# Kernel tuning notes

Measured on AMD Instinct MI355X. Metric: run time of the kernel, lower is better.

Reference implementation:

```python
import jax, jax.numpy as jnp
import numpy as np

B, T, D, H, C, WIN = 2, 2048, 512, 8, 64, 128
EPS = 1e-6


def _rms_norm(x, w):
    # x: (..., C)
    norm = jax.lax.rsqrt(jnp.mean(x * x, axis=-1, keepdims=True) + EPS)
    return x * norm * w


def _apply_rope(x, cos_p, sin_p):
    # x: (B, H, T, C); cos_p/sin_p: (T, C)
    half = x.shape[-1] // 2
    x1, x2 = x[..., :half], x[..., half:]
    rotated = jnp.concatenate([-x2, x1], axis=-1)
    return x * cos_p + rotated * sin_p


def setup_inputs() -> dict:
    key = jax.random.key(0)
    ks = jax.random.split(key, 5)
    h = jax.random.normal(ks[0], (B, T, D), dtype=jnp.float32)
    # RoPE cache (rotate-half convention): (T_max, head_dim)
    inv_freq = 1.0 / (10000.0 ** (jnp.arange(0, C, 2, dtype=jnp.float32) / C))  # (C/2,)
    pos = jnp.arange(T, dtype=jnp.float32)
    freqs = pos[:, None] * inv_freq[None, :]                      # (T, C/2)
    emb = jnp.concatenate([freqs, freqs], axis=-1)                # (T, C)
    rope_cos = jnp.cos(emb)
    rope_sin = jnp.sin(emb)
    scale = 0.02
    W_q = jax.random.normal(ks[1], (D, H * C), dtype=jnp.float32) * scale
    W_k = jax.random.normal(ks[2], (D, H * C), dtype=jnp.float32) * scale
    W_v = jax.random.normal(ks[3], (D, H * C), dtype=jnp.float32) * scale
    W_o = jax.random.normal(ks[4], (H * C, D), dtype=jnp.float32) * scale
    q_norm_w = jnp.ones((C,), dtype=jnp.float32)
    k_norm_w = jnp.ones((C,), dtype=jnp.float32)
    return {"h": h, "rope_cos": rope_cos, "rope_sin": rope_sin,
            "W_q": W_q, "W_k": W_k, "W_v": W_v, "W_o": W_o,
            "q_norm_w": q_norm_w, "k_norm_w": k_norm_w}


def reference(h, rope_cos, rope_sin, W_q, W_k, W_v, W_o, q_norm_w, k_norm_w):
    Bx, Tx, _ = h.shape
    q = (h @ W_q).reshape(Bx, Tx, H, C)
    k = (h @ W_k).reshape(Bx, Tx, H, C)
    v = (h @ W_v).reshape(Bx, Tx, H, C)
    q = _rms_norm(q, q_norm_w)
    k = _rms_norm(k, k_norm_w)
    positions = jnp.arange(Tx)
    cos_p = rope_cos[positions]   # (T, C)
    sin_p = rope_sin[positions]
    # transpose to (B, H, T, C), apply rope, transpose back handled implicitly
    q = _apply_rope(q.transpose(0, 2, 1, 3), cos_p, sin_p).transpose(0, 2, 1, 3)
    k = _apply_rope(k.transpose(0, 2, 1, 3), cos_p, sin_p).transpose(0, 2, 1, 3)
    i = positions[:, None]
    j = positions[None, :]
    sw_mask = (j <= i) & (j > i - WIN)                # (T, T) banded causal
    logits = jnp.einsum('bthc,bshc->bhts', q, k) / np.sqrt(C).astype(np.float32)
    logits = jnp.where(sw_mask[None, None], logits, jnp.float32(-jnp.inf))
    attn = jax.nn.softmax(logits, axis=-1)
    out = jnp.einsum('bhts,bshc->bthc', attn, v).reshape(Bx, Tx, H * C)
    return out @ W_o
```

## Files before the change

kernel.cpp:

```cpp
#include <hip/hip_runtime.h>
#include <hip/hip_bf16.h>
#include <cmath>

#define Bb 2
#define Tt 2048
#define Dd 512
#define Hh 8
#define Cc 64
#define WINw 128

using u16x8 = __attribute__((ext_vector_type(8))) unsigned short;
using s16x8 = __attribute__((ext_vector_type(8))) short;
using f32x4 = __attribute__((ext_vector_type(4))) float;

__device__ __forceinline__ float bf2f(unsigned short u) {
  union { unsigned int i; float f; } v; v.i = ((unsigned int)u) << 16; return v.f;
}
__device__ __forceinline__ unsigned short f2bf(float f) {
  __hip_bfloat16 b = __float2bfloat16(f);
  return *reinterpret_cast<unsigned short*>(&b);
}

#define GLD16(gp, lp)                                                        \
  __builtin_amdgcn_global_load_lds(                                          \
      (const __attribute__((address_space(1))) unsigned int*)(gp),           \
      (__attribute__((address_space(3))) unsigned int*)(lp), 16, 0, 0)

__global__ __launch_bounds__(256) void prep_all(
    const float* __restrict__ s0, const float* __restrict__ s1,
    const float* __restrict__ s2, const float* __restrict__ s3,
    unsigned short* __restrict__ d,
    const float* __restrict__ hsrc, unsigned short* __restrict__ hdst) {
  int tid = threadIdx.x;
  if (blockIdx.z == 4) {
    int gid = ((int)blockIdx.y * 8 + blockIdx.x) * 256 + tid;
    #pragma unroll
    for (int s = 0; s < 16; ++s) {
      size_t i = ((size_t)s * 16384 + gid) * 8;
      const float4* g = (const float4*)&hsrc[i];
      float4 f0 = g[0], f1 = g[1];
      u16x8 o = {f2bf(f0.x), f2bf(f0.y), f2bf(f0.z), f2bf(f0.w),
                 f2bf(f1.x), f2bf(f1.y), f2bf(f1.z), f2bf(f1.w)};
      *(u16x8*)&hdst[i] = o;
    }
    return;
  }
  __shared__ unsigned short tile[64 * 65];
  const float* srcs[4] = {s0, s1, s2, s3};
  const float* src = srcs[blockIdx.z];
  unsigned short* dst = d + (size_t)blockIdx.z * 512 * 512;
  int n0 = blockIdx.x * 64, k0 = blockIdx.y * 64;
  int tx = tid & 63, ty = tid >> 6;
  #pragma unroll
  for (int i = 0; i < 16; ++i) {
    int k = ty * 16 + i;
    tile[k * 65 + tx] = f2bf(src[(k0 + k) * 512 + n0 + tx]);
  }
  __syncthreads();
  #pragma unroll
  for (int i = 0; i < 16; ++i) {
    int n = ty * 16 + i;
    dst[(n0 + n) * 512 + k0 + tx] = tile[tx * 65 + n];
  }
}

__global__ __launch_bounds__(256) void qkv_fused(
    const unsigned short* __restrict__ Hb,
    const unsigned short* __restrict__ WTall,
    const float* __restrict__ qnw, const float* __restrict__ knw,
    const float* __restrict__ rcos, const float* __restrict__ rsin,
    unsigned short* __restrict__ Qw, unsigned short* __restrict__ Kw,
    unsigned short* __restrict__ Vw) {
  __shared__ alignas(16) unsigned short S[12288];
  unsigned short* Al = S;
  unsigned short* Bl = S + 8192;
  int tid = threadIdx.x;
  int wave = tid >> 6, lane = tid & 63;
  int ln = lane & 15, qd = lane >> 4;
  int m0 = blockIdx.x * 128;
  int gh = blockIdx.y;
  int n0 = gh * 64;

  f32x4 acc[2][4];
  #pragma unroll
  for (int mi = 0; mi < 2; ++mi)
    #pragma unroll
    for (int ni = 0; ni < 4; ++ni) acc[mi][ni] = f32x4{0.f, 0.f, 0.f, 0.f};

  for (int k0 = 0; k0 < 512; k0 += 64) {
    #pragma unroll
    for (int s = 0; s < 4; ++s) {
      int q = s * 4 + wave;
      int L = q * 64 + lane;
      int row = L >> 3;
      int cb = (L & 7) ^ (row & 7);
      GLD16(&Hb[(size_t)(m0 + row) * 512 + k0 + cb * 8], (char*)Al + q * 1024);
    }
    #pragma unroll
    for (int s = 0; s < 2; ++s) {
      int q = s * 4 + wave;
      int L = q * 64 + lane;
      int row = L >> 3;
      int cb = (L & 7) ^ (row & 7);
      GLD16(&WTall[(size_t)(n0 + row) * 512 + k0 + cb * 8], (char*)Bl + q * 1024);
    }
    __syncthreads();
    #pragma unroll
    for (int half = 0; half < 2; ++half) {
      s16x8 af[2], bfr[4];
      #pragma unroll
      for (int mi = 0; mi < 2; ++mi) {
        int ar = wave * 32 + mi * 16 + ln;
        int cbp = (qd + half * 4) ^ (ar & 7);
        af[mi] = *(const s16x8*)((const char*)Al + ar * 128 + cbp * 16);
      }
      #pragma unroll
      for (int ni = 0; ni < 4; ++ni) {
        int br = ni * 16 + ln;
        int cbp = (qd + half * 4) ^ (br & 7);
        bfr[ni] = *(const s16x8*)((const char*)Bl + br * 128 + cbp * 16);
      }
      #pragma unroll
      for (int mi = 0; mi < 2; ++mi)
        #pragma unroll
        for (int ni = 0; ni < 4; ++ni)
          acc[mi][ni] = __builtin_amdgcn_mfma_f32_16x16x32_bf16(
              af[mi], bfr[ni], acc[mi][ni], 0, 0, 0);
    }
    __syncthreads();
  }

  int mat = gh >> 3, head = gh & 7;
  const float* nw = (mat == 0) ? qnw : knw;
  bool do_rope = (mat < 2);
  int mrow0 = m0 + wave * 32;
  int b = mrow0 >> 11, tb = mrow0 & (Tt - 1);

  #pragma unroll
  for (int mi = 0; mi < 2; ++mi) {
    float vals[4][4];
    #pragma unroll
    for (int ni = 0; ni < 4; ++ni)
      #pragma unroll
      for (int r = 0; r < 4; ++r) vals[ni][r] = acc[mi][ni][r];

    if (do_rope) {
      #pragma unroll
      for (int r = 0; r < 4; ++r) {
        float ss = 0.f;
        #pragma unroll
        for (int ni = 0; ni < 4; ++ni) ss += vals[ni][r] * vals[ni][r];
        ss += __shfl_xor(ss, 1, 64);
        ss += __shfl_xor(ss, 2, 64);
        ss += __shfl_xor(ss, 4, 64);
        ss += __shfl_xor(ss, 8, 64);
        float nrm = rsqrtf(ss * (1.0f / 64.0f) + 1e-6f);
        #pragma unroll
        for (int ni = 0; ni < 4; ++ni) vals[ni][r] *= nrm;
      }
      #pragma unroll
      for (int ni = 0; ni < 4; ++ni) {
        float w = nw[ni * 16 + ln];
        #pragma unroll
        for (int r = 0; r < 4; ++r) vals[ni][r] *= w;
      }
      float res[4][4];
      #pragma unroll
      for (int r = 0; r < 4; ++r) {
        int t = tb + mi * 16 + qd * 4 + r;
        #pragma unroll
        for (int ni = 0; ni < 4; ++ni) {
          int c = ni * 16 + ln;
          float cs = rcos[t * 64 + c];
          float sn = rsin[t * 64 + c];
          float part = vals[ni ^ 2][r];
          float rot = (ni < 2) ? -part : part;
          res[ni][r] = vals[ni][r] * cs + rot * sn;
        }
      }
      #pragma unroll
      for (int ni = 0; ni < 4; ++ni)
        #pragma unroll
        for (int r = 0; r < 4; ++r) vals[ni][r] = res[ni][r];
    }

    if (mat < 2) {
      unsigned short* Wl = S + wave * 2304;
      #pragma unroll
      for (int ni = 0; ni < 4; ++ni)
        #pragma unroll
        for (int r = 0; r < 4; ++r)
          Wl[(mi * 16 + qd * 4 + r) * 72 + ni * 16 + ln] = f2bf(vals[ni][r]);
    } else {
      unsigned short* Wl = S + wave * 2560;
      #pragma unroll
      for (int ni = 0; ni < 4; ++ni)
        #pragma unroll
        for (int r = 0; r < 4; ++r)
          Wl[(ni * 16 + ln) * 40 + mi * 16 + qd * 4 + r] = f2bf(vals[ni][r]);
    }
  }

  if (mat < 2) {
    unsigned short* Wl = S + wave * 2304;
    unsigned short* Og =
        ((mat == 0) ? Qw : Kw) + (((size_t)b * Hh + head) * Tt + tb) * 64;
    #pragma unroll
    for (int i = 0; i < 4; ++i) {
      int idx = i * 64 + lane;
      int rr = idx >> 3, cc = (idx & 7) * 8;
      *(u16x8*)&Og[rr * 64 + cc] = *(const u16x8*)&Wl[rr * 72 + cc];
    }
  } else {
    unsigned short* Wl = S + wave * 2560;
    unsigned short* Og = Vw + ((size_t)b * Hh + head) * 64 * 2048 + tb;
    #pragma unroll
    for (int i = 0; i < 4; ++i) {
      int idx = i * 64 + lane;
      int rr = idx >> 2, cc = (idx & 3) * 8;
      *(u16x8*)&Og[(size_t)rr * 2048 + cc] = *(const u16x8*)&Wl[rr * 40 + cc];
    }
  }
}

__global__ __launch_bounds__(256) void attn_mfma(
    const unsigned short* __restrict__ Q,
    const unsigned short* __restrict__ K,
    const unsigned short* __restrict__ Vg,
    unsigned short* __restrict__ AO) {
  __shared__ alignas(16) unsigned short KP[192 * 72];
  __shared__ alignas(16) unsigned short Vt[64 * 200];
  int tid = threadIdx.x;
  int wave = tid >> 6, lane = tid & 63;
  int ln = lane & 15, qd = lane >> 4;
  int t0 = blockIdx.x * 64, bh = blockIdx.y;
  int kb = t0 - 128;
  int q0 = wave * 16;

  const unsigned short* Kg = K + (size_t)bh * Tt * 64;
  const unsigned short* Vb = Vg + (size_t)bh * 64 * 2048;

  int srow = tid >> 2, scol = (tid & 3) * 16;
  #pragma unroll
  for (int p = 0; p < 3; ++p) {
    int row = p * 64 + srow;
    int kg = kb + row; if (kg < 0) kg = 0;
    const u16x8* gk = (const u16x8*)&Kg[(size_t)kg * 64 + scol];
    u16x8 k0v = gk[0], k1v = gk[1];
    *(u16x8*)&KP[row * 72 + scol] = k0v;
    *(u16x8*)&KP[row * 72 + scol + 8] = k1v;
  }
  #pragma unroll
  for (int j = 0; j < 3; ++j)
    #pragma unroll
    for (int it = 0; it < 2; ++it) {
      int idx = it * 256 + tid;
      int row = idx >> 3, ch = (idx & 7) * 8;
      u16x8 v = *(const u16x8*)&Vb[(size_t)row * 2048 + kb + j * 64 + ch];
      *(u16x8*)&Vt[row * 200 + j * 64 + ch] = v;
    }
  const unsigned short* Qg = Q + ((size_t)bh * Tt + t0 + q0) * 64;
  s16x8 aq0 = *(const s16x8*)&Qg[ln * 64 + qd * 8];
  s16x8 aq1 = *(const s16x8*)&Qg[ln * 64 + 32 + qd * 8];
  __syncthreads();

  f32x4 sf[12];
  #pragma unroll
  for (int nt = 0; nt < 12; ++nt) {
    s16x8 b0 = *(const s16x8*)&KP[(nt * 16 + ln) * 72 + qd * 8];
    s16x8 b1 = *(const s16x8*)&KP[(nt * 16 + ln) * 72 + 32 + qd * 8];
    f32x4 a = {0.f, 0.f, 0.f, 0.f};
    a = __builtin_amdgcn_mfma_f32_16x16x32_bf16(aq0, b0, a, 0, 0, 0);
    a = __builtin_amdgcn_mfma_f32_16x16x32_bf16(aq1, b1, a, 0, 0, 0);
    sf[nt] = a;
  }
  __syncthreads();

  unsigned short* Pl = KP;
  int ok0 = (t0 < 128) ? (128 - t0) : 0;
  #pragma unroll
  for (int r = 0; r < 4; ++r) {
    int lq = q0 + qd * 4 + r;
    float mx = -INFINITY;
    #pragma unroll
    for (int nt = 0; nt < 12; ++nt) {
      int kk = nt * 16 + ln;
      bool valid = (kk > lq) && (kk <= lq + 128) && (kk >= ok0);
      float s = valid ? sf[nt][r] * 0.125f : -INFINITY;
      sf[nt][r] = s;
      mx = fmaxf(mx, s);
    }
    mx = fmaxf(mx, __shfl_xor(mx, 1, 64));
    mx = fmaxf(mx, __shfl_xor(mx, 2, 64));
    mx = fmaxf(mx, __shfl_xor(mx, 4, 64));
    mx = fmaxf(mx, __shfl_xor(mx, 8, 64));
    float sum = 0.f;
    #pragma unroll
    for (int nt = 0; nt < 12; ++nt) {
      float e = __expf(sf[nt][r] - mx);
      sf[nt][r] = e;
      sum += e;
    }
    sum += __shfl_xor(sum, 1, 64);
    sum += __shfl_xor(sum, 2, 64);
    sum += __shfl_xor(sum, 4, 64);
    sum += __shfl_xor(sum, 8, 64);
    float inv = 1.0f / sum;
    #pragma unroll
    for (int nt = 0; nt < 12; ++nt)
      Pl[lq * 200 + nt * 16 + ln] = f2bf(sf[nt][r] * inv);
  }

  f32x4 oa[4] = {f32x4{0,0,0,0}, f32x4{0,0,0,0}, f32x4{0,0,0,0}, f32x4{0,0,0,0}};
  #pragma unroll
  for (int s = 0; s < 6; ++s) {
    s16x8 ap = *(const s16x8*)&Pl[(q0 + ln) * 200 + s * 32 + qd * 8];
    #pragma unroll
    for (int nt = 0; nt < 4; ++nt) {
      s16x8 bv = *(const s16x8*)&Vt[(nt * 16 + ln) * 200 + s * 32 + qd * 8];
      oa[nt] = __builtin_amdgcn_mfma_f32_16x16x32_bf16(ap, bv, oa[nt], 0, 0, 0);
    }
  }

  unsigned short* Ow = KP + q0 * 200;
  #pragma unroll
  for (int ni = 0; ni < 4; ++ni)
    #pragma unroll
    for (int r = 0; r < 4; ++r)
      Ow[(qd * 4 + r) * 72 + ni * 16 + ln] = f2bf(oa[ni][r]);
  int b = bh >> 3, h = bh & 7;
  #pragma unroll
  for (int i = 0; i < 2; ++i) {
    int idx = i * 64 + lane;
    int rr = idx >> 3, cc = (idx & 7) * 8;
    *(u16x8*)&AO[((size_t)(b * Tt + t0 + q0 + rr) * Hh + h) * 64 + cc] =
        *(const u16x8*)&Ow[rr * 72 + cc];
  }
}

__global__ __launch_bounds__(256) void out_gemm(
    const unsigned short* __restrict__ Am,
    const unsigned short* __restrict__ WT,
    float* __restrict__ Out) {
  __shared__ alignas(16) unsigned short Al[64 * 64];
  __shared__ alignas(16) unsigned short Bl[64 * 64];
  int tid = threadIdx.x;
  int wave = tid >> 6, lane = tid & 63;
  int ln = lane & 15, qd = lane >> 4;
  int wm = wave >> 1, wn = wave & 1;
  int m0 = blockIdx.x * 64, n0 = blockIdx.y * 64;

  f32x4 acc[2][2];
  #pragma unroll
  for (int mi = 0; mi < 2; ++mi)
    #pragma unroll
    for (int ni = 0; ni < 2; ++ni) acc[mi][ni] = f32x4{0.f, 0.f, 0.f, 0.f};

  for (int k0 = 0; k0 < 512; k0 += 64) {
    #pragma unroll
    for (int s = 0; s < 2; ++s) {
      int q = s * 4 + wave;
      int L = q * 64 + lane;
      int row = L >> 3;
      int cb = (L & 7) ^ (row & 7);
      GLD16(&Am[(size_t)(m0 + row) * 512 + k0 + cb * 8], (char*)Al + q * 1024);
      GLD16(&WT[(size_t)(n0 + row) * 512 + k0 + cb * 8], (char*)Bl + q * 1024);
    }
    __syncthreads();
    #pragma unroll
    for (int half = 0; half < 2; ++half) {
      s16x8 af[2], bfr[2];
      #pragma unroll
      for (int mi = 0; mi < 2; ++mi) {
        int ar = wm * 32 + mi * 16 + ln;
        int cbp = (qd + half * 4) ^ (ar & 7);
        af[mi] = *(const s16x8*)((const char*)Al + ar * 128 + cbp * 16);
      }
      #pragma unroll
      for (int ni = 0; ni < 2; ++ni) {
        int br = wn * 32 + ni * 16 + ln;
        int cbp = (qd + half * 4) ^ (br & 7);
        bfr[ni] = *(const s16x8*)((const char*)Bl + br * 128 + cbp * 16);
      }
      #pragma unroll
      for (int mi = 0; mi < 2; ++mi)
        #pragma unroll
        for (int ni = 0; ni < 2; ++ni)
          acc[mi][ni] = __builtin_amdgcn_mfma_f32_16x16x32_bf16(
              af[mi], bfr[ni], acc[mi][ni], 0, 0, 0);
    }
    __syncthreads();
  }

  #pragma unroll
  for (int mi = 0; mi < 2; ++mi)
    #pragma unroll
    for (int r = 0; r < 4; ++r) {
      int row = m0 + wm * 32 + mi * 16 + qd * 4 + r;
      #pragma unroll
      for (int ni = 0; ni < 2; ++ni)
        Out[(size_t)row * 512 + n0 + wn * 32 + ni * 16 + ln] = acc[mi][ni][r];
    }
}

extern "C" void kernel_launch(void* const* d_in, const int* in_sizes, int n_in,
                              void* d_out, int out_size, void* d_ws, size_t ws_size,
                              hipStream_t stream) {
  const float* h   = (const float*)d_in[0];
  const float* rc  = (const float*)d_in[1];
  const float* rs  = (const float*)d_in[2];
  const float* Wq  = (const float*)d_in[3];
  const float* Wk  = (const float*)d_in[4];
  const float* Wv  = (const float*)d_in[5];
  const float* Wo  = (const float*)d_in[6];
  const float* qnw = (const float*)d_in[7];
  const float* knw = (const float*)d_in[8];

  unsigned short* ws    = (unsigned short*)d_ws;
  unsigned short* WTall = ws;
  unsigned short* WTo   = WTall + 1536 * 512;
  unsigned short* Hb    = WTo + 512 * 512;
  unsigned short* Qw    = Hb + 2097152;
  unsigned short* Kw    = Qw + 2097152;
  unsigned short* Vw    = Kw + 2097152;
  unsigned short* AOw   = Vw + 2097152;

  prep_all<<<dim3(8, 8, 5), 256, 0, stream>>>(Wq, Wk, Wv, Wo, WTall, h, Hb);

  qkv_fused<<<dim3(32, 24), 256, 0, stream>>>(Hb, WTall, qnw, knw, rc, rs,
                                              Qw, Kw, Vw);

  attn_mfma<<<dim3(32, 16), 256, 0, stream>>>(Qw, Kw, Vw, AOw);

  out_gemm<<<dim3(64, 8), 256, 0, stream>>>(AOw, WTo, (float*)d_out);
}
```

Measured before the change: 106.3 us.

## Fuse all stages into one persistent kernel with software grid barriers

Replaces the four kernel launches (weight/input conversion, QKV GEMM with norm+RoPE, windowed attention, output GEMM) with a single 512-block kernel that separates the phases with atomic-counter grid barriers, plus a memset to reset the counters. The goal is to remove launch gaps and per-kernel tail effects. The attention phase also stops staging V in LDS and reads V fragments straight from global memory. The grid barrier relies on all 512 blocks being resident at once (launch bounds of 2 blocks per CU), and its spin loop has a timeout break that could silently continue if that assumption fails.

```diff
diff --git a/kernel.cpp b/kernel.cpp
--- a/kernel.cpp
+++ b/kernel.cpp
@@ -4,18 +4,12 @@
 
 #define Bb 2
 #define Tt 2048
-#define Dd 512
 #define Hh 8
-#define Cc 64
-#define WINw 128
 
 using u16x8 = __attribute__((ext_vector_type(8))) unsigned short;
 using s16x8 = __attribute__((ext_vector_type(8))) short;
 using f32x4 = __attribute__((ext_vector_type(4))) float;
 
-__device__ __forceinline__ float bf2f(unsigned short u) {
-  union { unsigned int i; float f; } v; v.i = ((unsigned int)u) << 16; return v.f;
-}
 __device__ __forceinline__ unsigned short f2bf(float f) {
   __hip_bfloat16 b = __float2bfloat16(f);
   return *reinterpret_cast<unsigned short*>(&b);
@@ -26,386 +20,394 @@
       (const __attribute__((address_space(1))) unsigned int*)(gp),           \
       (__attribute__((address_space(3))) unsigned int*)(lp), 16, 0, 0)
 
-__global__ __launch_bounds__(256) void prep_all(
-    const float* __restrict__ s0, const float* __restrict__ s1,
-    const float* __restrict__ s2, const float* __restrict__ s3,
-    unsigned short* __restrict__ d,
-    const float* __restrict__ hsrc, unsigned short* __restrict__ hdst) {
+__device__ __forceinline__ void gbar(unsigned int* c, unsigned int target) {
+  __syncthreads();
+  if (threadIdx.x == 0) {
+    __threadfence();
+    __hip_atomic_fetch_add(c, 1u, __ATOMIC_RELEASE, __HIP_MEMORY_SCOPE_AGENT);
+    int guard = 0;
+    while (__hip_atomic_load(c, __ATOMIC_ACQUIRE, __HIP_MEMORY_SCOPE_AGENT) <
+           target) {
+      __builtin_amdgcn_s_sleep(4);
+      if (++guard > (1 << 24)) break;
+    }
+    __threadfence();
+  }
+  __syncthreads();
+}
+
+__global__ __launch_bounds__(256, 2) void mega(
+    const float* __restrict__ h, const float* __restrict__ rcos,
+    const float* __restrict__ rsin,
+    const float* __restrict__ W0, const float* __restrict__ W1,
+    const float* __restrict__ W2, const float* __restrict__ W3,
+    const float* __restrict__ qnw, const float* __restrict__ knw,
+    unsigned short* __restrict__ WTall,
+    unsigned short* __restrict__ Hb,
+    unsigned short* __restrict__ Qw,
+    unsigned short* __restrict__ Kw,
+    unsigned short* __restrict__ Vw,
+    unsigned short* __restrict__ AOw,
+    float* __restrict__ Out,
+    unsigned int* __restrict__ ctr) {
+  __shared__ alignas(16) unsigned short S[13824];
   int tid = threadIdx.x;
-  if (blockIdx.z == 4) {
-    int gid = ((int)blockIdx.y * 8 + blockIdx.x) * 256 + tid;
-    #pragma unroll
-    for (int s = 0; s < 16; ++s) {
-      size_t i = ((size_t)s * 16384 + gid) * 8;
-      const float4* g = (const float4*)&hsrc[i];
+  int bid = blockIdx.x;
+  int wave = tid >> 6, lane = tid & 63;
+  int ln = lane & 15, qd = lane >> 4;
+
+  if (bid < 256) {
+    const float* srcs[4] = {W0, W1, W2, W3};
+    const float* src = srcs[bid >> 6];
+    unsigned short* dst = WTall + (size_t)(bid >> 6) * 512 * 512;
+    int tl = bid & 63;
+    int n0 = (tl & 7) * 64, k0 = (tl >> 3) * 64;
+    int tx = tid & 63, ty = tid >> 6;
+    #pragma unroll
+    for (int i = 0; i < 16; ++i) {
+      int k = ty * 16 + i;
+      S[k * 65 + tx] = f2bf(src[(k0 + k) * 512 + n0 + tx]);
+    }
+    __syncthreads();
+    #pragma unroll
+    for (int i = 0; i < 16; ++i) {
+      int n = ty * 16 + i;
+      dst[(n0 + n) * 512 + k0 + tx] = S[tx * 65 + n];
+    }
+  } else {
+    size_t base = (size_t)(bid - 256) * 8192;
+    #pragma unroll
+    for (int s = 0; s < 4; ++s) {
+      size_t i = base + s * 2048 + tid * 8;
+      const float4* g = (const float4*)&h[i];
       float4 f0 = g[0], f1 = g[1];
       u16x8 o = {f2bf(f0.x), f2bf(f0.y), f2bf(f0.z), f2bf(f0.w),
                  f2bf(f1.x), f2bf(f1.y), f2bf(f1.z), f2bf(f1.w)};
-      *(u16x8*)&hdst[i] = o;
-    }
-    return;
+      *(u16x8*)&Hb[i] = o;
+    }
   }
-  __shared__ unsigned short tile[64 * 65];
-  const float* srcs[4] = {s0, s1, s2, s3};
-  const float* src = srcs[blockIdx.z];
-  unsigned short* dst = d + (size_t)blockIdx.z * 512 * 512;
-  int n0 = blockIdx.x * 64, k0 = blockIdx.y * 64;
-  int tx = tid & 63, ty = tid >> 6;
-  #pragma unroll
-  for (int i = 0; i < 16; ++i) {
-    int k = ty * 16 + i;
-    tile[k * 65 + tx] = f2bf(src[(k0 + k) * 512 + n0 + tx]);
+  gbar(ctr + 0, 512);
+
+  for (int t = bid; t < 768; t += 512) {
+    int m0 = (t & 31) * 128;
+    int gh = t >> 5;
+    int n0 = gh * 64;
+    unsigned short* Al = S;
+    unsigned short* Bl = S + 8192;
+    __syncthreads();
+
+    f32x4 acc[2][4];
+    #pragma unroll
+    for (int mi = 0; mi < 2; ++mi)
+      #pragma unroll
+      for (int ni = 0; ni < 4; ++ni) acc[mi][ni] = f32x4{0.f, 0.f, 0.f, 0.f};
+
+    for (int k0 = 0; k0 < 512; k0 += 64) {
+      #pragma unroll
+      for (int s = 0; s < 4; ++s) {
+        int q = s * 4 + wave;
+        int L = q * 64 + lane;
+        int row = L >> 3;
+        int cb = (L & 7) ^ (row & 7);
+        GLD16(&Hb[(size_t)(m0 + row) * 512 + k0 + cb * 8], (char*)Al + q * 1024);
+      }
+      #pragma unroll
+      for (int s = 0; s < 2; ++s) {
+        int q = s * 4 + wave;
+        int L = q * 64 + lane;
+        int row = L >> 3;
+        int cb = (L & 7) ^ (row & 7);
+        GLD16(&WTall[(size_t)(n0 + row) * 512 + k0 + cb * 8],
+              (char*)Bl + q * 1024);
+      }
+      __syncthreads();
+      #pragma unroll
+      for (int half = 0; half < 2; ++half) {
+        s16x8 af[2], bfr[4];
+        #pragma unroll
+        for (int mi = 0; mi < 2; ++mi) {
+          int ar = wave * 32 + mi * 16 + ln;
+          int cbp = (qd + half * 4) ^ (ar & 7);
+          af[mi] = *(const s16x8*)((const char*)Al + ar * 128 + cbp * 16);
+        }
+        #pragma unroll
+        for (int ni = 0; ni < 4; ++ni) {
+          int br = ni * 16 + ln;
+          int cbp = (qd + half * 4) ^ (br & 7);
+          bfr[ni] = *(const s16x8*)((const char*)Bl + br * 128 + cbp * 16);
+        }
+        #pragma unroll
+        for (int mi = 0; mi < 2; ++mi)
+          #pragma unroll
+          for (int ni = 0; ni < 4; ++ni)
+            acc[mi][ni] = __builtin_amdgcn_mfma_f32_16x16x32_bf16(
+                af[mi], bfr[ni], acc[mi][ni], 0, 0, 0);
+      }
+      __syncthreads();
+    }
+
+    int mat = gh >> 3, head = gh & 7;
+    const float* nw = (mat == 0) ? qnw : knw;
+    bool do_rope = (mat < 2);
+    int mrow0 = m0 + wave * 32;
+    int b = mrow0 >> 11, tb = mrow0 & (Tt - 1);
+
+    #pragma unroll
+    for (int mi = 0; mi < 2; ++mi) {
+      float vals[4][4];
+      #pragma unroll
+      for (int ni = 0; ni < 4; ++ni)
+        #pragma unroll
+        for (int r = 0; r < 4; ++r) vals[ni][r] = acc[mi][ni][r];
+
+      if (do_rope) {
+        #pragma unroll
+        for (int r = 0; r < 4; ++r) {
+          float ss = 0.f;
+          #pragma unroll
+          for (int ni = 0; ni < 4; ++ni) ss += vals[ni][r] * vals[ni][r];
+          ss += __shfl_xor(ss, 1, 64);
+          ss += __shfl_xor(ss, 2, 64);
+          ss += __shfl_xor(ss, 4, 64);
+          ss += __shfl_xor(ss, 8, 64);
+          float nrm = rsqrtf(ss * (1.0f / 64.0f) + 1e-6f);
+          #pragma unroll
+          for (int ni = 0; ni < 4; ++ni) vals[ni][r] *= nrm;
+        }
+        #pragma unroll
+        for (int ni = 0; ni < 4; ++ni) {
+          float w = nw[ni * 16 + ln];
+          #pragma unroll
+          for (int r = 0; r < 4; ++r) vals[ni][r] *= w;
+        }
+        float res[4][4];
+        #pragma unroll
+        for (int r = 0; r < 4; ++r) {
+          int tt = tb + mi * 16 + qd * 4 + r;
+          #pragma unroll
+          for (int ni = 0; ni < 4; ++ni) {
+            int c = ni * 16 + ln;
+            float cs = rcos[tt * 64 + c];
+            float sn = rsin[tt * 64 + c];
+            float part = vals[ni ^ 2][r];
+            float rot = (ni < 2) ? -part : part;
+            res[ni][r] = vals[ni][r] * cs + rot * sn;
+          }
+        }
+        #pragma unroll
+        for (int ni = 0; ni < 4; ++ni)
+          #pragma unroll
+          for (int r = 0; r < 4; ++r) vals[ni][r] = res[ni][r];
+      }
+
+      if (mat < 2) {
+        unsigned short* Wl = S + wave * 2304;
+        #pragma unroll
+        for (int ni = 0; ni < 4; ++ni)
+          #pragma unroll
+          for (int r = 0; r < 4; ++r)
+            Wl[(mi * 16 + qd * 4 + r) * 72 + ni * 16 + ln] = f2bf(vals[ni][r]);
+      } else {
+        unsigned short* Wl = S + wave * 2560;
+        #pragma unroll
+        for (int ni = 0; ni < 4; ++ni)
+          #pragma unroll
+          for (int r = 0; r < 4; ++r)
+            Wl[(ni * 16 + ln) * 40 + mi * 16 + qd * 4 + r] = f2bf(vals[ni][r]);
+      }
+    }
+
+    if (mat < 2) {
+      unsigned short* Wl = S + wave * 2304;
+      unsigned short* Og =
+          ((mat == 0) ? Qw : Kw) + (((size_t)b * Hh + head) * Tt + tb) * 64;
+      #pragma unroll
+      for (int i = 0; i < 4; ++i) {
+        int idx = i * 64 + lane;
+        int rr = idx >> 3, cc = (idx & 7) * 8;
+        *(u16x8*)&Og[rr * 64 + cc] = *(const u16x8*)&Wl[rr * 72 + cc];
+      }
+    } else {
+      unsigned short* Wl = S + wave * 2560;
+      unsigned short* Og = Vw + ((size_t)b * Hh + head) * 64 * 2048 + tb;
+      #pragma unroll
+      for (int i = 0; i < 4; ++i) {
+        int idx = i * 64 + lane;
+        int rr = idx >> 2, cc = (idx & 3) * 8;
+        *(u16x8*)&Og[(size_t)rr * 2048 + cc] = *(const u16x8*)&Wl[rr * 40 + cc];
+      }
+    }
   }
-  __syncthreads();
-  #pragma unroll
-  for (int i = 0; i < 16; ++i) {
-    int n = ty * 16 + i;
-    dst[(n0 + n) * 512 + k0 + tx] = tile[tx * 65 + n];
+  gbar(ctr + 1, 512);
+
+  {
+    int t0 = (bid & 31) * 64;
+    int bh = bid >> 5;
+    int kb = t0 - 128;
+    int q0 = wave * 16;
+    const unsigned short* Kg = Kw + (size_t)bh * Tt * 64;
+    const unsigned short* Vb = Vw + (size_t)bh * 64 * 2048;
+    unsigned short* KP = S;
+    __syncthreads();
+
+    int srow = tid >> 2, scol = (tid & 3) * 16;
+    #pragma unroll
+    for (int p = 0; p < 3; ++p) {
+      int row = p * 64 + srow;
+      int kg = kb + row; if (kg < 0) kg = 0;
+      const u16x8* gk = (const u16x8*)&Kg[(size_t)kg * 64 + scol];
+      u16x8 k0v = gk[0], k1v = gk[1];
+      *(u16x8*)&KP[row * 72 + scol] = k0v;
+      *(u16x8*)&KP[row * 72 + scol + 8] = k1v;
+    }
+    const unsigned short* Qg = Qw + ((size_t)bh * Tt + t0 + q0) * 64;
+    s16x8 aq0 = *(const s16x8*)&Qg[ln * 64 + qd * 8];
+    s16x8 aq1 = *(const s16x8*)&Qg[ln * 64 + 32 + qd * 8];
+    __syncthreads();
+
+    f32x4 sf[12];
+    #pragma unroll
+    for (int nt = 0; nt < 12; ++nt) {
+      s16x8 b0 = *(const s16x8*)&KP[(nt * 16 + ln) * 72 + qd * 8];
+      s16x8 b1 = *(const s16x8*)&KP[(nt * 16 + ln) * 72 + 32 + qd * 8];
+      f32x4 a = {0.f, 0.f, 0.f, 0.f};
+      a = __builtin_amdgcn_mfma_f32_16x16x32_bf16(aq0, b0, a, 0, 0, 0);
+      a = __builtin_amdgcn_mfma_f32_16x16x32_bf16(aq1, b1, a, 0, 0, 0);
+      sf[nt] = a;
+    }
+    __syncthreads();
+
+    unsigned short* Pl = KP;
+    int ok0 = (t0 < 128) ? (128 - t0) : 0;
+    #pragma unroll
+    for (int r = 0; r < 4; ++r) {
+      int lq = q0 + qd * 4 + r;
+      float mx = -INFINITY;
+      #pragma unroll
+      for (int nt = 0; nt < 12; ++nt) {
+        int kk = nt * 16 + ln;
+        bool valid = (kk > lq) && (kk <= lq + 128) && (kk >= ok0);
+        float s = valid ? sf[nt][r] * 0.125f : -INFINITY;
+        sf[nt][r] = s;
+        mx = fmaxf(mx, s);
+      }
+      mx = fmaxf(mx, __shfl_xor(mx, 1, 64));
+      mx = fmaxf(mx, __shfl_xor(mx, 2, 64));
+      mx = fmaxf(mx, __shfl_xor(mx, 4, 64));
+      mx = fmaxf(mx, __shfl_xor(mx, 8, 64));
+      float sum = 0.f;
+      #pragma unroll
+      for (int nt = 0; nt < 12; ++nt) {
+        float e = __expf(sf[nt][r] - mx);
+        sf[nt][r] = e;
+        sum += e;
+      }
+      sum += __shfl_xor(sum, 1, 64);
+      sum += __shfl_xor(sum, 2, 64);
+      sum += __shfl_xor(sum, 4, 64);
+      sum += __shfl_xor(sum, 8, 64);
+      float inv = 1.0f / sum;
+      #pragma unroll
+      for (int nt = 0; nt < 12; ++nt)
+        Pl[lq * 200 + nt * 16 + ln] = f2bf(sf[nt][r] * inv);
+    }
+
+    f32x4 oa[4] = {f32x4{0,0,0,0}, f32x4{0,0,0,0}, f32x4{0,0,0,0},
+                   f32x4{0,0,0,0}};
+    #pragma unroll
+    for (int s = 0; s < 6; ++s) {
+      s16x8 ap = *(const s16x8*)&Pl[(q0 + ln) * 200 + s * 32 + qd * 8];
+      #pragma unroll
+      for (int nt = 0; nt < 4; ++nt) {
+        s16x8 bv = *(const s16x8*)&Vb[(size_t)(nt * 16 + ln) * 2048 + kb +
+                                      s * 32 + qd * 8];
+        oa[nt] = __builtin_amdgcn_mfma_f32_16x16x32_bf16(ap, bv, oa[nt], 0, 0, 0);
+      }
+    }
+
+    unsigned short* Ow = KP + q0 * 200;
+    #pragma unroll
+    for (int ni = 0; ni < 4; ++ni)
+      #pragma unroll
+      for (int r = 0; r < 4; ++r)
+        Ow[(qd * 4 + r) * 72 + ni * 16 + ln] = f2bf(oa[ni][r]);
+    int b = bh >> 3, hh = bh & 7;
+    #pragma unroll
+    for (int i = 0; i < 2; ++i) {
+      int idx = i * 64 + lane;
+      int rr = idx >> 3, cc = (idx & 7) * 8;
+      *(u16x8*)&AOw[((size_t)(b * Tt + t0 + q0 + rr) * Hh + hh) * 64 + cc] =
+          *(const u16x8*)&Ow[rr * 72 + cc];
+    }
+  }
+  gbar(ctr + 2, 512);
+
+  {
+    int m0 = (bid & 63) * 64;
+    int n0 = (bid >> 6) * 64;
+    const unsigned short* WTo = WTall + (size_t)3 * 512 * 512;
+    unsigned short* Al = S;
+    unsigned short* Bl = S + 4096;
+    int wm = wave >> 1, wn = wave & 1;
+    __syncthreads();
+
+    f32x4 acc[2][2];
+    #pragma unroll
+    for (int mi = 0; mi < 2; ++mi)
+      #pragma unroll
+      for (int ni = 0; ni < 2; ++ni) acc[mi][ni] = f32x4{0.f, 0.f, 0.f, 0.f};
+
+    for (int k0 = 0; k0 < 512; k0 += 64) {
+      #pragma unroll
+      for (int s = 0; s < 2; ++s) {
+        int q = s * 4 + wave;
+        int L = q * 64 + lane;
+        int row = L >> 3;
+        int cb = (L & 7) ^ (row & 7);
+        GLD16(&AOw[(size_t)(m0 + row) * 512 + k0 + cb * 8], (char*)Al + q * 1024);
+        GLD16(&WTo[(size_t)(n0 + row) * 512 + k0 + cb * 8], (char*)Bl + q * 1024);
+      }
+      __syncthreads();
+      #pragma unroll
+      for (int half = 0; half < 2; ++half) {
+        s16x8 af[2], bfr[2];
+        #pragma unroll
+        for (int mi = 0; mi < 2; ++mi) {
+          int ar = wm * 32 + mi * 16 + ln;
+          int cbp = (qd + half * 4) ^ (ar & 7);
+          af[mi] = *(const s16x8*)((const char*)Al + ar * 128 + cbp * 16);
+        }
+        #pragma unroll
+        for (int ni = 0; ni < 2; ++ni) {
+          int br = wn * 32 + ni * 16 + ln;
+          int cbp = (qd + half * 4) ^ (br & 7);
+          bfr[ni] = *(const s16x8*)((const char*)Bl + br * 128 + cbp * 16);
+        }
+        #pragma unroll
+        for (int mi = 0; mi < 2; ++mi)
+          #pragma unroll
+          for (int ni = 0; ni < 2; ++ni)
+            acc[mi][ni] = __builtin_amdgcn_mfma_f32_16x16x32_bf16(
+                af[mi], bfr[ni], acc[mi][ni], 0, 0, 0);
+      }
+      __syncthreads();
+    }
+
+    #pragma unroll
+    for (int mi = 0; mi < 2; ++mi)
+      #pragma unroll
+      for (int r = 0; r < 4; ++r) {
+        int row = m0 + wm * 32 + mi * 16 + qd * 4 + r;
+        #pragma unroll
+        for (int ni = 0; ni < 2; ++ni)
+          Out[(size_t)row * 512 + n0 + wn * 32 + ni * 16 + ln] = acc[mi][ni][r];
+      }
   }
 }
 
-__global__ __launch_bounds__(256) void qkv_fused(
-    const unsigned short* __restrict__ Hb,
-    const unsigned short* __restrict__ WTall,
-    const float* __restrict__ qnw, const float* __restrict__ knw,
-    const float* __restrict__ rcos, const float* __restrict__ rsin,
-    unsigned short* __restrict__ Qw, unsigned short* __restrict__ Kw,
-    unsigned short* __restrict__ Vw) {
-  __shared__ alignas(16) unsigned short S[12288];
-  unsigned short* Al = S;
-  unsigned short* Bl = S + 8192;
-  int tid = threadIdx.x;
-  int wave = tid >> 6, lane = tid & 63;
-  int ln = lane & 15, qd = lane >> 4;
-  int m0 = blockIdx.x * 128;
-  int gh = blockIdx.y;
-  int n0 = gh * 64;
-
-  f32x4 acc[2][4];
-  #pragma unroll
-  for (int mi = 0; mi < 2; ++mi)
-    #pragma unroll
-    for (int ni = 0; ni < 4; ++ni) acc[mi][ni] = f32x4{0.f, 0.f, 0.f, 0.f};
-
-  for (int k0 = 0; k0 < 512; k0 += 64) {
-    #pragma unroll
-    for (int s = 0; s < 4; ++s) {
-      int q = s * 4 + wave;
-      int L = q * 64 + lane;
-      int row = L >> 3;
-      int cb = (L & 7) ^ (row & 7);
-      GLD16(&Hb[(size_t)(m0 + row) * 512 + k0 + cb * 8], (char*)Al + q * 1024);
-    }
-    #pragma unroll
-    for (int s = 0; s < 2; ++s) {
-      int q = s * 4 + wave;
-      int L = q * 64 + lane;
-      int row = L >> 3;
-      int cb = (L & 7) ^ (row & 7);
-      GLD16(&WTall[(size_t)(n0 + row) * 512 + k0 + cb * 8], (char*)Bl + q * 1024);
-    }
-    __syncthreads();
-    #pragma unroll
-    for (int half = 0; half < 2; ++half) {
-      s16x8 af[2], bfr[4];
-      #pragma unroll
-      for (int mi = 0; mi < 2; ++mi) {
-        int ar = wave * 32 + mi * 16 + ln;
-        int cbp = (qd + half * 4) ^ (ar & 7);
-        af[mi] = *(const s16x8*)((const char*)Al + ar * 128 + cbp * 16);
-      }
-      #pragma unroll
-      for (int ni = 0; ni < 4; ++ni) {
-        int br = ni * 16 + ln;
-        int cbp = (qd + half * 4) ^ (br & 7);
-        bfr[ni] = *(const s16x8*)((const char*)Bl + br * 128 + cbp * 16);
-      }
-      #pragma unroll
-      for (int mi = 0; mi < 2; ++mi)
-        #pragma unroll
-        for (int ni = 0; ni < 4; ++ni)
-          acc[mi][ni] = __builtin_amdgcn_mfma_f32_16x16x32_bf16(
-              af[mi], bfr[ni], acc[mi][ni], 0, 0, 0);
-    }
-    __syncthreads();
-  }
-
-  int mat = gh >> 3, head = gh & 7;
-  const float* nw = (mat == 0) ? qnw : knw;
-  bool do_rope = (mat < 2);
-  int mrow0 = m0 + wave * 32;
-  int b = mrow0 >> 11, tb = mrow0 & (Tt - 1);
-
-  #pragma unroll
-  for (int mi = 0; mi < 2; ++mi) {
-    float vals[4][4];
-    #pragma unroll
-    for (int ni = 0; ni < 4; ++ni)
-      #pragma unroll
-      for (int r = 0; r < 4; ++r) vals[ni][r] = acc[mi][ni][r];
-
-    if (do_rope) {
-      #pragma unroll
-      for (int r = 0; r < 4; ++r) {
-        float ss = 0.f;
-        #pragma unroll
-        for (int ni = 0; ni < 4; ++ni) ss += vals[ni][r] * vals[ni][r];
-        ss += __shfl_xor(ss, 1, 64);
-        ss += __shfl_xor(ss, 2, 64);
-        ss += __shfl_xor(ss, 4, 64);
-        ss += __shfl_xor(ss, 8, 64);
-        float nrm = rsqrtf(ss * (1.0f / 64.0f) + 1e-6f);
-        #pragma unroll
-        for (int ni = 0; ni < 4; ++ni) vals[ni][r] *= nrm;
-      }
-      #pragma unroll
-      for (int ni = 0; ni < 4; ++ni) {
-        float w = nw[ni * 16 + ln];
-        #pragma unroll
-        for (int r = 0; r < 4; ++r) vals[ni][r] *= w;
-      }
-      float res[4][4];
-      #pragma unroll
-      for (int r = 0; r < 4; ++r) {
-        int t = tb + mi * 16 + qd * 4 + r;
-        #pragma unroll
-        for (int ni = 0; ni < 4; ++ni) {
-          int c = ni * 16 + ln;
-          float cs = rcos[t * 64 + c];
-          float sn = rsin[t * 64 + c];
-          float part = vals[ni ^ 2][r];
-          float rot = (ni < 2) ? -part : part;
-          res[ni][r] = vals[ni][r] * cs + rot * sn;
-        }
-      }
-      #pragma unroll
-      for (int ni = 0; ni < 4; ++ni)
-        #pragma unroll
-        for (int r = 0; r < 4; ++r) vals[ni][r] = res[ni][r];
-    }
-
-    if (mat < 2) {
-      unsigned short* Wl = S + wave * 2304;
-      #pragma unroll
-      for (int ni = 0; ni < 4; ++ni)
-        #pragma unroll
-        for (int r = 0; r < 4; ++r)
-          Wl[(mi * 16 + qd * 4 + r) * 72 + ni * 16 + ln] = f2bf(vals[ni][r]);
-    } else {
-      unsigned short* Wl = S + wave * 2560;
-      #pragma unroll
-      for (int ni = 0; ni < 4; ++ni)
-        #pragma unroll
-        for (int r = 0; r < 4; ++r)
-          Wl[(ni * 16 + ln) * 40 + mi * 16 + qd * 4 + r] = f2bf(vals[ni][r]);
-    }
-  }
-
-  if (mat < 2) {
-    unsigned short* Wl = S + wave * 2304;
-    unsigned short* Og =
-        ((mat == 0) ? Qw : Kw) + (((size_t)b * Hh + head) * Tt + tb) * 64;
-    #pragma unroll
-    for (int i = 0; i < 4; ++i) {
-      int idx = i * 64 + lane;
-      int rr = idx >> 3, cc = (idx & 7) * 8;
-      *(u16x8*)&Og[rr * 64 + cc] = *(const u16x8*)&Wl[rr * 72 + cc];
-    }
-  } else {
-    unsigned short* Wl = S + wave * 2560;
-    unsigned short* Og = Vw + ((size_t)b * Hh + head) * 64 * 2048 + tb;
-    #pragma unroll
-    for (int i = 0; i < 4; ++i) {
-      int idx = i * 64 + lane;
-      int rr = idx >> 2, cc = (idx & 3) * 8;
-      *(u16x8*)&Og[(size_t)rr * 2048 + cc] = *(const u16x8*)&Wl[rr * 40 + cc];
-    }
-  }
-}
-
-__global__ __launch_bounds__(256) void attn_mfma(
-    const unsigned short* __restrict__ Q,
-    const unsigned short* __restrict__ K,
-    const unsigned short* __restrict__ Vg,
-    unsigned short* __restrict__ AO) {
-  __shared__ alignas(16) unsigned short KP[192 * 72];
-  __shared__ alignas(16) unsigned short Vt[64 * 200];
-  int tid = threadIdx.x;
-  int wave = tid >> 6, lane = tid & 63;
-  int ln = lane & 15, qd = lane >> 4;
-  int t0 = blockIdx.x * 64, bh = blockIdx.y;
-  int kb = t0 - 128;
-  int q0 = wave * 16;
-
-  const unsigned short* Kg = K + (size_t)bh * Tt * 64;
-  const unsigned short* Vb = Vg + (size_t)bh * 64 * 2048;
-
-  int srow = tid >> 2, scol = (tid & 3) * 16;
-  #pragma unroll
-  for (int p = 0; p < 3; ++p) {
-    int row = p * 64 + srow;
-    int kg = kb + row; if (kg < 0) kg = 0;
-    const u16x8* gk = (const u16x8*)&Kg[(size_t)kg * 64 + scol];
-    u16x8 k0v = gk[0], k1v = gk[1];
-    *(u16x8*)&KP[row * 72 + scol] = k0v;
-    *(u16x8*)&KP[row * 72 + scol + 8] = k1v;
-  }
-  #pragma unroll
-  for (int j = 0; j < 3; ++j)
-    #pragma unroll
-    for (int it = 0; it < 2; ++it) {
-      int idx = it * 256 + tid;
-      int row = idx >> 3, ch = (idx & 7) * 8;
-      u16x8 v = *(const u16x8*)&Vb[(size_t)row * 2048 + kb + j * 64 + ch];
-      *(u16x8*)&Vt[row * 200 + j * 64 + ch] = v;
-    }
-  const unsigned short* Qg = Q + ((size_t)bh * Tt + t0 + q0) * 64;
-  s16x8 aq0 = *(const s16x8*)&Qg[ln * 64 + qd * 8];
-  s16x8 aq1 = *(const s16x8*)&Qg[ln * 64 + 32 + qd * 8];
-  __syncthreads();
-
-  f32x4 sf[12];
-  #pragma unroll
-  for (int nt = 0; nt < 12; ++nt) {
-    s16x8 b0 = *(const s16x8*)&KP[(nt * 16 + ln) * 72 + qd * 8];
-    s16x8 b1 = *(const s16x8*)&KP[(nt * 16 + ln) * 72 + 32 + qd * 8];
-    f32x4 a = {0.f, 0.f, 0.f, 0.f};
-    a = __builtin_amdgcn_mfma_f32_16x16x32_bf16(aq0, b0, a, 0, 0, 0);
-    a = __builtin_amdgcn_mfma_f32_16x16x32_bf16(aq1, b1, a, 0, 0, 0);
-    sf[nt] = a;
-  }
-  __syncthreads();
-
-  unsigned short* Pl = KP;
-  int ok0 = (t0 < 128) ? (128 - t0) : 0;
-  #pragma unroll
-  for (int r = 0; r < 4; ++r) {
-    int lq = q0 + qd * 4 + r;
-    float mx = -INFINITY;
-    #pragma unroll
-    for (int nt = 0; nt < 12; ++nt) {
-      int kk = nt * 16 + ln;
-      bool valid = (kk > lq) && (kk <= lq + 128) && (kk >= ok0);
-      float s = valid ? sf[nt][r] * 0.125f : -INFINITY;
-      sf[nt][r] = s;
-      mx = fmaxf(mx, s);
-    }
-    mx = fmaxf(mx, __shfl_xor(mx, 1, 64));
-    mx = fmaxf(mx, __shfl_xor(mx, 2, 64));
-    mx = fmaxf(mx, __shfl_xor(mx, 4, 64));
-    mx = fmaxf(mx, __shfl_xor(mx, 8, 64));
-    float sum = 0.f;
-    #pragma unroll
-    for (int nt = 0; nt < 12; ++nt) {
-      float e = __expf(sf[nt][r] - mx);
-      sf[nt][r] = e;
-      sum += e;
-    }
-    sum += __shfl_xor(sum, 1, 64);
-    sum += __shfl_xor(sum, 2, 64);
-    sum += __shfl_xor(sum, 4, 64);
-    sum += __shfl_xor(sum, 8, 64);
-    float inv = 1.0f / sum;
-    #pragma unroll
-    for (int nt = 0; nt < 12; ++nt)
-      Pl[lq * 200 + nt * 16 + ln] = f2bf(sf[nt][r] * inv);
-  }
-
-  f32x4 oa[4] = {f32x4{0,0,0,0}, f32x4{0,0,0,0}, f32x4{0,0,0,0}, f32x4{0,0,0,0}};
-  #pragma unroll
-  for (int s = 0; s < 6; ++s) {
-    s16x8 ap = *(const s16x8*)&Pl[(q0 + ln) * 200 + s * 32 + qd * 8];
-    #pragma unroll
-    for (int nt = 0; nt < 4; ++nt) {
-      s16x8 bv = *(const s16x8*)&Vt[(nt * 16 + ln) * 200 + s * 32 + qd * 8];
-      oa[nt] = __builtin_amdgcn_mfma_f32_16x16x32_bf16(ap, bv, oa[nt], 0, 0, 0);
-    }
-  }
-
-  unsigned short* Ow = KP + q0 * 200;
-  #pragma unroll
-  for (int ni = 0; ni < 4; ++ni)
-    #pragma unroll
-    for (int r = 0; r < 4; ++r)
-      Ow[(qd * 4 + r) * 72 + ni * 16 + ln] = f2bf(oa[ni][r]);
-  int b = bh >> 3, h = bh & 7;
-  #pragma unroll
-  for (int i = 0; i < 2; ++i) {
-    int idx = i * 64 + lane;
-    int rr = idx >> 3, cc = (idx & 7) * 8;
-    *(u16x8*)&AO[((size_t)(b * Tt + t0 + q0 + rr) * Hh + h) * 64 + cc] =
-        *(const u16x8*)&Ow[rr * 72 + cc];
-  }
-}
-
-__global__ __launch_bounds__(256) void out_gemm(
-    const unsigned short* __restrict__ Am,
-    const unsigned short* __restrict__ WT,
-    float* __restrict__ Out) {
-  __shared__ alignas(16) unsigned short Al[64 * 64];
-  __shared__ alignas(16) unsigned short Bl[64 * 64];
-  int tid = threadIdx.x;
-  int wave = tid >> 6, lane = tid & 63;
-  int ln = lane & 15, qd = lane >> 4;
-  int wm = wave >> 1, wn = wave & 1;
-  int m0 = blockIdx.x * 64, n0 = blockIdx.y * 64;
-
-  f32x4 acc[2][2];
-  #pragma unroll
-  for (int mi = 0; mi < 2; ++mi)
-    #pragma unroll
-    for (int ni = 0; ni < 2; ++ni) acc[mi][ni] = f32x4{0.f, 0.f, 0.f, 0.f};
-
-  for (int k0 = 0; k0 < 512; k0 += 64) {
-    #pragma unroll
-    for (int s = 0; s < 2; ++s) {
-      int q = s * 4 + wave;
-      int L = q * 64 + lane;
-      int row = L >> 3;
-      int cb = (L & 7) ^ (row & 7);
-      GLD16(&Am[(size_t)(m0 + row) * 512 + k0 + cb * 8], (char*)Al + q * 1024);
-      GLD16(&WT[(size_t)(n0 + row) * 512 + k0 + cb * 8], (char*)Bl + q * 1024);
-    }
-    __syncthreads();
-    #pragma unroll
-    for (int half = 0; half < 2; ++half) {
-      s16x8 af[2], bfr[2];
-      #pragma unroll
-      for (int mi = 0; mi < 2; ++mi) {
-        int ar = wm * 32 + mi * 16 + ln;
-        int cbp = (qd + half * 4) ^ (ar & 7);
-        af[mi] = *(const s16x8*)((const char*)Al + ar * 128 + cbp * 16);
-      }
-      #pragma unroll
-      for (int ni = 0; ni < 2; ++ni) {
-        int br = wn * 32 + ni * 16 + ln;
-        int cbp = (qd + half * 4) ^ (br & 7);
-        bfr[ni] = *(const s16x8*)((const char*)Bl + br * 128 + cbp * 16);
-      }
-      #pragma unroll
-      for (int mi = 0; mi < 2; ++mi)
-        #pragma unroll
-        for (int ni = 0; ni < 2; ++ni)
-          acc[mi][ni] = __builtin_amdgcn_mfma_f32_16x16x32_bf16(
-              af[mi], bfr[ni], acc[mi][ni], 0, 0, 0);
-    }
-    __syncthreads();
-  }
-
-  #pragma unroll
-  for (int mi = 0; mi < 2; ++mi)
-    #pragma unroll
-    for (int r = 0; r < 4; ++r) {
-      int row = m0 + wm * 32 + mi * 16 + qd * 4 + r;
-      #pragma unroll
-      for (int ni = 0; ni < 2; ++ni)
-        Out[(size_t)row * 512 + n0 + wn * 32 + ni * 16 + ln] = acc[mi][ni][r];
-    }
-}
-
 extern "C" void kernel_launch(void* const* d_in, const int* in_sizes, int n_in,
-                              void* d_out, int out_size, void* d_ws, size_t ws_size,
-                              hipStream_t stream) {
+                              void* d_out, int out_size, void* d_ws,
+                              size_t ws_size, hipStream_t stream) {
   const float* h   = (const float*)d_in[0];
   const float* rc  = (const float*)d_in[1];
   const float* rs  = (const float*)d_in[2];
@@ -418,19 +420,15 @@
 
   unsigned short* ws    = (unsigned short*)d_ws;
   unsigned short* WTall = ws;
-  unsigned short* WTo   = WTall + 1536 * 512;
-  unsigned short* Hb    = WTo + 512 * 512;
+  unsigned short* Hb    = WTall + 4 * 512 * 512;
   unsigned short* Qw    = Hb + 2097152;
   unsigned short* Kw    = Qw + 2097152;
   unsigned short* Vw    = Kw + 2097152;
   unsigned short* AOw   = Vw + 2097152;
-
-  prep_all<<<dim3(8, 8, 5), 256, 0, stream>>>(Wq, Wk, Wv, Wo, WTall, h, Hb);
-
-  qkv_fused<<<dim3(32, 24), 256, 0, stream>>>(Hb, WTall, qnw, knw, rc, rs,
-                                              Qw, Kw, Vw);
-
-  attn_mfma<<<dim3(32, 16), 256, 0, stream>>>(Qw, Kw, Vw, AOw);
-
-  out_gemm<<<dim3(64, 8), 256, 0, stream>>>(AOw, WTo, (float*)d_out);
+  unsigned int*   ctr   = (unsigned int*)((char*)d_ws + (64u << 20));
+
+  hipMemsetAsync(ctr, 0, 64, stream);
+  mega<<<512, 256, 0, stream>>>(h, rc, rs, Wq, Wk, Wv, Wo, qnw, knw,
+                                WTall, Hb, Qw, Kw, Vw, AOw,
+                                (float*)d_out, ctr);
 }
```

Measured after the change: 339.2 us. 3.19x slower.

## Double-buffer LDS tiles in QKV and output GEMMs to overlap loads with MFMA

Applied to the files above, without the earlier changes.

The QKV projection and output projection GEMMs now keep two LDS buffers. Each iteration issues the global-to-LDS copies for the next K-slice before running the MFMAs on the current one, and the separate post-load barrier is dropped. This is meant to hide global load latency behind matrix math and cut barriers per iteration. In exchange the kernels use twice the shared memory, which may lower occupancy. Correctness relies on the remaining end-of-iteration barrier waiting for the async LDS loads to finish.

```diff
diff --git a/kernel.cpp b/kernel.cpp
--- a/kernel.cpp
+++ b/kernel.cpp
@@ -2,20 +2,13 @@
 #include <hip/hip_bf16.h>
 #include <cmath>
 
-#define Bb 2
 #define Tt 2048
-#define Dd 512
 #define Hh 8
-#define Cc 64
-#define WINw 128
 
 using u16x8 = __attribute__((ext_vector_type(8))) unsigned short;
 using s16x8 = __attribute__((ext_vector_type(8))) short;
 using f32x4 = __attribute__((ext_vector_type(4))) float;
 
-__device__ __forceinline__ float bf2f(unsigned short u) {
-  union { unsigned int i; float f; } v; v.i = ((unsigned int)u) << 16; return v.f;
-}
 __device__ __forceinline__ unsigned short f2bf(float f) {
   __hip_bfloat16 b = __float2bfloat16(f);
   return *reinterpret_cast<unsigned short*>(&b);
@@ -71,9 +64,7 @@
     const float* __restrict__ rcos, const float* __restrict__ rsin,
     unsigned short* __restrict__ Qw, unsigned short* __restrict__ Kw,
     unsigned short* __restrict__ Vw) {
-  __shared__ alignas(16) unsigned short S[12288];
-  unsigned short* Al = S;
-  unsigned short* Bl = S + 8192;
+  __shared__ alignas(16) unsigned short S[24576];
   int tid = threadIdx.x;
   int wave = tid >> 6, lane = tid & 63;
   int ln = lane & 15, qd = lane >> 4;
@@ -87,14 +78,16 @@
     #pragma unroll
     for (int ni = 0; ni < 4; ++ni) acc[mi][ni] = f32x4{0.f, 0.f, 0.f, 0.f};
 
-  for (int k0 = 0; k0 < 512; k0 += 64) {
+  auto stage = [&](int k0, int buf) {
+    char* Apt = (char*)(S + buf * 12288);
+    char* Bpt = (char*)(S + buf * 12288 + 8192);
     #pragma unroll
     for (int s = 0; s < 4; ++s) {
       int q = s * 4 + wave;
       int L = q * 64 + lane;
       int row = L >> 3;
       int cb = (L & 7) ^ (row & 7);
-      GLD16(&Hb[(size_t)(m0 + row) * 512 + k0 + cb * 8], (char*)Al + q * 1024);
+      GLD16(&Hb[(size_t)(m0 + row) * 512 + k0 + cb * 8], Apt + q * 1024);
     }
     #pragma unroll
     for (int s = 0; s < 2; ++s) {
@@ -102,9 +95,17 @@
       int L = q * 64 + lane;
       int row = L >> 3;
       int cb = (L & 7) ^ (row & 7);
-      GLD16(&WTall[(size_t)(n0 + row) * 512 + k0 + cb * 8], (char*)Bl + q * 1024);
-    }
-    __syncthreads();
+      GLD16(&WTall[(size_t)(n0 + row) * 512 + k0 + cb * 8], Bpt + q * 1024);
+    }
+  };
+
+  stage(0, 0);
+  __syncthreads();
+  for (int it = 0; it < 8; ++it) {
+    int cur = it & 1;
+    if (it < 7) stage((it + 1) * 64, cur ^ 1);
+    const char* Al = (const char*)(S + cur * 12288);
+    const char* Bl = (const char*)(S + cur * 12288 + 8192);
     #pragma unroll
     for (int half = 0; half < 2; ++half) {
       s16x8 af[2], bfr[4];
@@ -112,13 +113,13 @@
       for (int mi = 0; mi < 2; ++mi) {
         int ar = wave * 32 + mi * 16 + ln;
         int cbp = (qd + half * 4) ^ (ar & 7);
-        af[mi] = *(const s16x8*)((const char*)Al + ar * 128 + cbp * 16);
+        af[mi] = *(const s16x8*)(Al + ar * 128 + cbp * 16);
       }
       #pragma unroll
       for (int ni = 0; ni < 4; ++ni) {
         int br = ni * 16 + ln;
         int cbp = (qd + half * 4) ^ (br & 7);
-        bfr[ni] = *(const s16x8*)((const char*)Bl + br * 128 + cbp * 16);
+        bfr[ni] = *(const s16x8*)(Bl + br * 128 + cbp * 16);
       }
       #pragma unroll
       for (int mi = 0; mi < 2; ++mi)
@@ -342,8 +343,7 @@
     const unsigned short* __restrict__ Am,
     const unsigned short* __restrict__ WT,
     float* __restrict__ Out) {
-  __shared__ alignas(16) unsigned short Al[64 * 64];
-  __shared__ alignas(16) unsigned short Bl[64 * 64];
+  __shared__ alignas(16) unsigned short S[16384];
   int tid = threadIdx.x;
   int wave = tid >> 6, lane = tid & 63;
   int ln = lane & 15, qd = lane >> 4;
@@ -356,17 +356,27 @@
     #pragma unroll
     for (int ni = 0; ni < 2; ++ni) acc[mi][ni] = f32x4{0.f, 0.f, 0.f, 0.f};
 
-  for (int k0 = 0; k0 < 512; k0 += 64) {
+  auto stage = [&](int k0, int buf) {
+    char* Apt = (char*)(S + buf * 8192);
+    char* Bpt = (char*)(S + buf * 8192 + 4096);
     #pragma unroll
     for (int s = 0; s < 2; ++s) {
       int q = s * 4 + wave;
       int L = q * 64 + lane;
       int row = L >> 3;
       int cb = (L & 7) ^ (row & 7);
-      GLD16(&Am[(size_t)(m0 + row) * 512 + k0 + cb * 8], (char*)Al + q * 1024);
-      GLD16(&WT[(size_t)(n0 + row) * 512 + k0 + cb * 8], (char*)Bl + q * 1024);
-    }
-    __syncthreads();
+      GLD16(&Am[(size_t)(m0 + row) * 512 + k0 + cb * 8], Apt + q * 1024);
+      GLD16(&WT[(size_t)(n0 + row) * 512 + k0 + cb * 8], Bpt + q * 1024);
+    }
+  };
+
+  stage(0, 0);
+  __syncthreads();
+  for (int it = 0; it < 8; ++it) {
+    int cur = it & 1;
+    if (it < 7) stage((it + 1) * 64, cur ^ 1);
+    const char* Al = (const char*)(S + cur * 8192);
+    const char* Bl = (const char*)(S + cur * 8192 + 4096);
     #pragma unroll
     for (int half = 0; half < 2; ++half) {
       s16x8 af[2], bfr[2];
@@ -374,13 +384,13 @@
       for (int mi = 0; mi < 2; ++mi) {
         int ar = wm * 32 + mi * 16 + ln;
         int cbp = (qd + half * 4) ^ (ar & 7);
-        af[mi] = *(const s16x8*)((const char*)Al + ar * 128 + cbp * 16);
+        af[mi] = *(const s16x8*)(Al + ar * 128 + cbp * 16);
       }
       #pragma unroll
       for (int ni = 0; ni < 2; ++ni) {
         int br = wn * 32 + ni * 16 + ln;
         int cbp = (qd + half * 4) ^ (br & 7);
-        bfr[ni] = *(const s16x8*)((const char*)Bl + br * 128 + cbp * 16);
+        bfr[ni] = *(const s16x8*)(Bl + br * 128 + cbp * 16);
       }
       #pragma unroll
       for (int mi = 0; mi < 2; ++mi)
@@ -404,8 +414,8 @@
 }
 
 extern "C" void kernel_launch(void* const* d_in, const int* in_sizes, int n_in,
-                              void* d_out, int out_size, void* d_ws, size_t ws_size,
-                              hipStream_t stream) {
+                              void* d_out, int out_size, void* d_ws,
+                              size_t ws_size, hipStream_t stream) {
   const float* h   = (const float*)d_in[0];
   const float* rc  = (const float*)d_in[1];
   const float* rs  = (const float*)d_in[2];
```

New measurement: 106.1 us. Within noise of the previous version (-0.2%).
